# Kernel tuning notes

Measured on AMD Instinct MI355X. Metric: run time of the kernel, lower is better.

The kernel has to match this reference:

```python
import jax, jax.numpy as jnp
import numpy as np

B, C_IN, C_OUT, H, W = 4, 256, 256, 64, 64
K, STRIDE, PAD, DIL = 3, 1, 1, 1
KK = K * K


def setup_inputs() -> dict:
    key = jax.random.key(0)
    k1, k2, k3, k4 = jax.random.split(key, 4)
    x = jax.random.normal(k1, (B, C_IN, H, W), jnp.float32)
    # offset/mask conv weight (no bias), scaled small so offsets are modest
    w_mod = jax.random.normal(k2, (3 * KK, C_IN, K, K), jnp.float32) * 0.01
    # deform conv weight (xavier-ish scale) + bias
    w_def = jax.random.normal(k3, (C_OUT, C_IN, K, K), jnp.float32) * (1.0 / np.sqrt(C_IN * KK))
    b_def = jax.random.normal(k4, (C_OUT,), jnp.float32) * 0.01
    return {"x": x, "w_mod": w_mod, "w_def": w_def, "b_def": b_def}


def _conv_nchw(x, w, stride, pad):
    return jax.lax.conv_general_dilated(
        x, w, (stride, stride), [(pad, pad), (pad, pad)],
        dimension_numbers=("NCHW", "OIHW", "NCHW"))


def _bilinear_sample(x, py, px):
    # x: [B,C,H,W]; py/px: [B,KK,Ho,Wo] absolute sample coords (zero-pad outside)
    Bn, Cc, Hh, Ww = x.shape
    y0 = jnp.floor(py)
    x0 = jnp.floor(px)
    fy = py - y0
    fx = px - x0
    y0i = y0.astype(jnp.int32)
    x0i = x0.astype(jnp.int32)
    xf = x.reshape(Bn, Cc, Hh * Ww)

    def corner(yi, xi, wgt):
        valid = (yi >= 0) & (yi < Hh) & (xi >= 0) & (xi < Ww)
        yc = jnp.clip(yi, 0, Hh - 1)
        xc = jnp.clip(xi, 0, Ww - 1)
        idx = yc * Ww + xc                      # [B,KK,Ho,Wo]
        g = jax.vmap(lambda f, i: f[:, i])(xf, idx)  # [B,C,KK,Ho,Wo]
        return g * (wgt * valid)[:, None]

    return (corner(y0i, x0i, (1 - fy) * (1 - fx))
            + corner(y0i, x0i + 1, (1 - fy) * fx)
            + corner(y0i + 1, x0i, fy * (1 - fx))
            + corner(y0i + 1, x0i + 1, fy * fx))


def reference(x, w_mod, w_def, b_def):
    # offset/mask head
    mod = _conv_nchw(x, w_mod, STRIDE, PAD)          # [B, 3*KK, Ho, Wo]
    o1, o2, mask = mod[:, :KK], mod[:, KK:2 * KK], mod[:, 2 * KK:]
    offset = jnp.concatenate([o1, o2], axis=1)        # [B, 2*KK, Ho, Wo]
    # torchvision DeformConv2d: offset channels are interleaved (y, x) pairs
    dy = offset[:, 0::2]
    dx = offset[:, 1::2]
    mask = jax.nn.sigmoid(mask)                       # [B, KK, Ho, Wo]

    Ho, Wo = mod.shape[2], mod.shape[3]
    ky, kx = jnp.meshgrid(jnp.arange(K), jnp.arange(K), indexing="ij")
    ky = ky.reshape(-1).astype(jnp.float32)
    kx = kx.reshape(-1).astype(jnp.float32)
    base_y = (jnp.arange(Ho, dtype=jnp.float32) * STRIDE - PAD)[None, :, None] + (ky * DIL)[:, None, None]  # [KK,Ho,1]
    base_x = (jnp.arange(Wo, dtype=jnp.float32) * STRIDE - PAD)[None, None, :] + (kx * DIL)[:, None, None]  # [KK,1,Wo]
    py = dy + base_y[None]                            # [B,KK,Ho,Wo]
    px = dx + base_x[None]

    sampled = _bilinear_sample(x, py, px) * mask[:, None]  # [B,C,KK,Ho,Wo]
    out = jnp.einsum("bckhw,ock->bohw", sampled, w_def.reshape(C_OUT, C_IN, KK))
    return out + b_def[None, :, None, None]
```

## Files before the change

kernel.cpp:

```cpp
#include <hip/hip_runtime.h>

typedef unsigned short u16;
typedef unsigned int u32;
typedef short bf16x8 __attribute__((ext_vector_type(8)));
typedef float f32x4 __attribute__((ext_vector_type(4)));

#define CIN 256
#define COUT 256

__device__ __forceinline__ u16 f2b(float f) {
  u32 u = __float_as_uint(f);
  u += 0x7fffu + ((u >> 16) & 1u);
  return (u16)(u >> 16);
}
__device__ __forceinline__ u32 packbf(float lo, float hi) {
  return (u32)f2b(lo) | ((u32)f2b(hi) << 16);
}
__device__ __forceinline__ u32 bil2(u32 u00, u32 u01, u32 u10, u32 u11, float4 wt) {
  float s0 = __uint_as_float(u00 << 16) * wt.x;
  s0 = fmaf(__uint_as_float(u01 << 16), wt.y, s0);
  s0 = fmaf(__uint_as_float(u10 << 16), wt.z, s0);
  s0 = fmaf(__uint_as_float(u11 << 16), wt.w, s0);
  float s1 = __uint_as_float(u00 & 0xffff0000u) * wt.x;
  s1 = fmaf(__uint_as_float(u01 & 0xffff0000u), wt.y, s1);
  s1 = fmaf(__uint_as_float(u10 & 0xffff0000u), wt.z, s1);
  s1 = fmaf(__uint_as_float(u11 & 0xffff0000u), wt.w, s1);
  return packbf(s0, s1);
}
__device__ __forceinline__ void bar() {
  asm volatile("s_waitcnt lgkmcnt(0)\n\ts_barrier" ::: "memory");
}

__global__ __launch_bounds__(256) void k_prep(
    const float* __restrict__ x, const float* __restrict__ w_mod,
    const float* __restrict__ w_def,
    u16* __restrict__ xT, u16* __restrict__ Wm2, u16* __restrict__ W2) {
  __shared__ __align__(16) char SB[9216];
  int t = threadIdx.x, g = blockIdx.x;
  if (g < 1024) {
    u16 (*T)[72] = (u16(*)[72])SB;
    int b = g >> 8, ct = (g >> 6) & 3, pt = g & 63;
    int c0 = ct << 6, pos0 = pt << 6;
    {
      int cl = t >> 2, pb = (t & 3) << 4;
      const float* p = x + (((b << 8) + c0 + cl) << 12) + pos0 + pb;
#pragma unroll
      for (int i = 0; i < 4; ++i) {
        float4 v = *(const float4*)(p + i * 4);
        int pp = pb + i * 4;
        T[pp][cl] = f2b(v.x); T[pp + 1][cl] = f2b(v.y);
        T[pp + 2][cl] = f2b(v.z); T[pp + 3][cl] = f2b(v.w);
      }
    }
    __syncthreads();
    {
      int pl = t >> 2, q = t & 3;
      u16* dst = xT + (((b << 12) + pos0 + pl) << 8) + c0 + (q << 4);
      *(uint4*)dst = *(const uint4*)&T[pl][q << 4];
      *(uint4*)(dst + 8) = *(const uint4*)&T[pl][(q << 4) + 8];
    }
  } else {
    float* L = (float*)SB;
    int gg = g - 1024;
    if (gg < 256) {
      const float* src = w_def + gg * 2304;
      for (int j = t; j < 2304; j += 256) L[j] = src[j];
      __syncthreads();
      u16* dst = W2 + gg * 2304;
      for (int j = t; j < 2304; j += 256) {
        int kk = j >> 8, c = j & 255;
        dst[j] = f2b(L[c * 9 + kk]);
      }
    } else {
      int cm = gg - 256;
      if (cm < 27) {
        const float* src = w_mod + cm * 2304;
        for (int j = t; j < 2304; j += 256) L[j] = src[j];
      }
      __syncthreads();
      u16* dst = Wm2 + cm * 2304;
      for (int j = t; j < 2304; j += 256) {
        int kk = j >> 8, c = j & 255;
        dst[j] = (cm < 27) ? f2b(L[c * 9 + kk]) : (u16)0;
      }
    }
  }
}

__global__ __launch_bounds__(1024) void k_fused(
    const u16* __restrict__ xT, const u16* __restrict__ Wm2,
    const u16* __restrict__ W2, const float* __restrict__ b_def,
    float* __restrict__ out) {
  __shared__ __align__(16) char LB[107520];
  __shared__ __align__(16) int2 Ci[576];
  __shared__ __align__(16) float4 Cw[576];
  u16 (*As1)[2][64][72] = (u16 (*)[2][64][72])LB;
  float (*mods2)[32][66] = (float (*)[32][66])(LB + 73728);
  u16 (*As2)[64][72] = (u16 (*)[64][72])LB;

  int t = threadIdx.x;
  int l = t & 63;
  int w = t >> 6;
  int g = blockIdx.x;
  int b = (g & 7) >> 1, y = ((g >> 3) << 1) + (g & 1);
  const u16* xTb = xT + (b << 20);
  int ml = l & 15, kq = l >> 4;

  {
    int h = t >> 8;
    int wl = (t >> 6) & 3;
    int tg = t & 255;
    int px = tg >> 2, q = tg & 3;
    f32x4 zero = {0.f, 0.f, 0.f, 0.f};
    f32x4 acc0 = zero, acc1 = zero;
    uint4 VA0, VA1, VB0, VB1;
    uint4 S0, S1, S2, S3, T0, T1, T2, T3;

#define MC_ISSUE_A(i, V0, V1)                                                \
  { int ch_ = h * 9 + (i); int kk_ = ch_ >> 2, c0_ = (ch_ & 3) << 6;         \
    int ky_ = kk_ / 3, kx_ = kk_ - 3 * ky_;                                  \
    int ys_ = y + ky_ - 1, xs_ = px + kx_ - 1;                               \
    V0 = make_uint4(0, 0, 0, 0); V1 = V0;                                    \
    if (ys_ >= 0 && ys_ < 64 && xs_ >= 0 && xs_ < 64) {                      \
      const u16* p_ = xTb + (((ys_ << 6) + xs_) << 8) + c0_ + (q << 4);      \
      V0 = *(const uint4*)p_; V1 = *(const uint4*)(p_ + 8);                  \
    } }

#define MC_ISSUE_B(i, R0, R1, R2, R3)                                        \
  { int ch_ = h * 9 + (i); int kk_ = ch_ >> 2, c0_ = (ch_ & 3) << 6;         \
    const u16* pw_ = Wm2 + (kk_ << 8) + c0_ + (kq << 3);                     \
    R0 = *(const uint4*)(pw_ + ml * 2304);                                   \
    R1 = *(const uint4*)(pw_ + (16 + ml) * 2304);                            \
    R2 = *(const uint4*)(pw_ + ml * 2304 + 32);                              \
    R3 = *(const uint4*)(pw_ + (16 + ml) * 2304 + 32); }

#define MC_WRITE(buf, V0, V1)                                                \
  { *(uint4*)&As1[h][buf][px][q << 4] = V0;                                  \
    *(uint4*)&As1[h][buf][px][(q << 4) + 8] = V1; }

#define MC_MFMA(buf, R0, R1, R2, R3)                                         \
  { bf16x8 a0_ = *(const bf16x8*)&As1[h][buf][wl * 16 + ml][kq << 3];        \
    acc0 = __builtin_amdgcn_mfma_f32_16x16x32_bf16(a0_, *(const bf16x8*)&R0, acc0, 0,0,0); \
    acc1 = __builtin_amdgcn_mfma_f32_16x16x32_bf16(a0_, *(const bf16x8*)&R1, acc1, 0,0,0); \
    bf16x8 a1_ = *(const bf16x8*)&As1[h][buf][wl * 16 + ml][32 + (kq << 3)]; \
    acc0 = __builtin_amdgcn_mfma_f32_16x16x32_bf16(a1_, *(const bf16x8*)&R2, acc0, 0,0,0); \
    acc1 = __builtin_amdgcn_mfma_f32_16x16x32_bf16(a1_, *(const bf16x8*)&R3, acc1, 0,0,0); }

    MC_ISSUE_A(0, VA0, VA1)
    MC_ISSUE_A(1, VB0, VB1)
    MC_ISSUE_B(0, S0, S1, S2, S3)
#pragma unroll 1
    for (int i2 = 0; i2 < 8; i2 += 2) {
      MC_WRITE(0, VA0, VA1)
      bar();
      MC_ISSUE_A(i2 + 2, VA0, VA1)
      MC_ISSUE_B(i2 + 1, T0, T1, T2, T3)
      MC_MFMA(0, S0, S1, S2, S3)
      MC_WRITE(1, VB0, VB1)
      bar();
      if (i2 + 3 < 9) MC_ISSUE_A(i2 + 3, VB0, VB1)
      MC_ISSUE_B(i2 + 2, S0, S1, S2, S3)
      MC_MFMA(1, T0, T1, T2, T3)
    }
    MC_WRITE(0, VA0, VA1)
    bar();
    MC_MFMA(0, S0, S1, S2, S3)
#pragma unroll
    for (int r = 0; r < 4; ++r) {
      mods2[h][ml][wl * 16 + kq * 4 + r]      = acc0[r];
      mods2[h][16 + ml][wl * 16 + kq * 4 + r] = acc1[r];
    }
#undef MC_ISSUE_A
#undef MC_ISSUE_B
#undef MC_WRITE
#undef MC_MFMA
  }
  __syncthreads();
  if (t < 576) {
    int kk = t >> 6, pxx_i = t & 63;
    float dy = mods2[0][2 * kk][pxx_i] + mods2[1][2 * kk][pxx_i]
             + mods2[2][2 * kk][pxx_i] + mods2[3][2 * kk][pxx_i];
    float dx = mods2[0][2 * kk + 1][pxx_i] + mods2[1][2 * kk + 1][pxx_i]
             + mods2[2][2 * kk + 1][pxx_i] + mods2[3][2 * kk + 1][pxx_i];
    float mv = mods2[0][18 + kk][pxx_i] + mods2[1][18 + kk][pxx_i]
             + mods2[2][18 + kk][pxx_i] + mods2[3][18 + kk][pxx_i];
    float msk = 1.f / (1.f + __expf(-mv));
    int ky = kk / 3, kx = kk - 3 * ky;
    float py  = dy + (float)(y + ky - 1);
    float pxx = dx + (float)(pxx_i + kx - 1);
    float y0f = floorf(py), x0f = floorf(pxx);
    float fy = py - y0f, fx = pxx - x0f;
    int y0 = (int)y0f, x0 = (int)x0f;
    float vy0 = (y0 >= 0 && y0 < 64) ? msk : 0.f;
    float vy1 = (y0 + 1 >= 0 && y0 + 1 < 64) ? msk : 0.f;
    float w00 = (1.f - fy) * (1.f - fx) * vy0;
    float w01 = (1.f - fy) * fx * vy0;
    float w10 = fy * (1.f - fx) * vy1;
    float w11 = fy * fx * vy1;
    int xb2 = min(max(x0, 0), 62);
    float wA0 = (xb2 == x0) ? w00 : ((xb2 == x0 + 1) ? w01 : 0.f);
    float wB0 = (xb2 + 1 == x0) ? w00 : ((xb2 + 1 == x0 + 1) ? w01 : 0.f);
    float wA1 = (xb2 == x0) ? w10 : ((xb2 == x0 + 1) ? w11 : 0.f);
    float wB1 = (xb2 + 1 == x0) ? w10 : ((xb2 + 1 == x0 + 1) ? w11 : 0.f);
    int ib0 = min(max(y0, 0), 63) * 64 + xb2;
    int ib1 = min(max(y0 + 1, 0), 63) * 64 + xb2;
    Ci[t] = make_int2(ib0, ib1);
    Cw[t] = make_float4(wA0, wB0, wA1, wB1);
  }
  __syncthreads();

  {
    int cp = t >> 9;
    int gm = (t >> 3) & 63, go = t & 7;
    int nrow0 = (w << 4) + ml;

    f32x4 zero = {0.f, 0.f, 0.f, 0.f};
    f32x4 acc[4];
#pragma unroll
    for (int i = 0; i < 4; ++i) acc[i] = zero;

    uint4 A00, A01, A02, A03; float4 wt0;
    uint4 A10, A11, A12, A13; float4 wt1;
    uint4 SA0, SA2;
    uint4 SB0, SB2;
    uint4 TA0, TA2;
    uint4 TB0, TB2;

#define ISSUE_A(chunk, a0, a1, a2, a3, wt)                                   \
  { int kk_ = (chunk) >> 2, c0_ = ((chunk) & 3) << 6;                        \
    int cI_ = (kk_ << 6) + gm;                                               \
    int2 ib_ = Ci[cI_];                                                      \
    wt = Cw[cI_];                                                            \
    const u16* p0_ = xTb + (ib_.x << 8) + c0_ + (go << 3);                   \
    const u16* p1_ = xTb + (ib_.y << 8) + c0_ + (go << 3);                   \
    a0 = *(const uint4*)p0_;  a1 = *(const uint4*)(p0_ + 256);               \
    a2 = *(const uint4*)p1_;  a3 = *(const uint4*)(p1_ + 256); }

#define ISSUE_B(chunk, R0, R2)                                               \
  { int kk_ = (chunk) >> 2, c0_ = ((chunk) & 3) << 6;                        \
    const u16* pw_ = W2 + (kk_ << 8) + c0_ + (kq << 3);                      \
    R0 = *(const uint4*)(pw_ + nrow0 * 2304);                                \
    R2 = *(const uint4*)(pw_ + nrow0 * 2304 + 32); }

#define UNPACK(CUR, a0, a1, a2, a3, wt)                                      \
  { u32 q0_ = bil2(a0.x, a1.x, a2.x, a3.x, wt);                              \
    u32 q1_ = bil2(a0.y, a1.y, a2.y, a3.y, wt);                              \
    u32 q2_ = bil2(a0.z, a1.z, a2.z, a3.z, wt);                              \
    u32 q3_ = bil2(a0.w, a1.w, a2.w, a3.w, wt);                              \
    *(uint4*)&As2[CUR][gm][go << 3] = make_uint4(q0_, q1_, q2_, q3_); }

#define DOMFMA(CUR, R0, R2)                                                  \
  { bf16x8 a0_ = *(const bf16x8*)&As2[CUR][ml][kq << 3];                     \
    bf16x8 a1_ = *(const bf16x8*)&As2[CUR][16 + ml][kq << 3];                \
    bf16x8 a2_ = *(const bf16x8*)&As2[CUR][32 + ml][kq << 3];                \
    bf16x8 a3_ = *(const bf16x8*)&As2[CUR][48 + ml][kq << 3];                \
    bf16x8 b0_ = *(const bf16x8*)&R0;                                        \
    acc[0] = __builtin_amdgcn_mfma_f32_16x16x32_bf16(a0_, b0_, acc[0], 0,0,0); \
    acc[1] = __builtin_amdgcn_mfma_f32_16x16x32_bf16(a1_, b0_, acc[1], 0,0,0); \
    acc[2] = __builtin_amdgcn_mfma_f32_16x16x32_bf16(a2_, b0_, acc[2], 0,0,0); \
    acc[3] = __builtin_amdgcn_mfma_f32_16x16x32_bf16(a3_, b0_, acc[3], 0,0,0); \
    a0_ = *(const bf16x8*)&As2[CUR][ml][32 + (kq << 3)];                     \
    a1_ = *(const bf16x8*)&As2[CUR][16 + ml][32 + (kq << 3)];                \
    a2_ = *(const bf16x8*)&As2[CUR][32 + ml][32 + (kq << 3)];                \
    a3_ = *(const bf16x8*)&As2[CUR][48 + ml][32 + (kq << 3)];                \
    b0_ = *(const bf16x8*)&R2;                                               \
    acc[0] = __builtin_amdgcn_mfma_f32_16x16x32_bf16(a0_, b0_, acc[0], 0,0,0); \
    acc[1] = __builtin_amdgcn_mfma_f32_16x16x32_bf16(a1_, b0_, acc[1], 0,0,0); \
    acc[2] = __builtin_amdgcn_mfma_f32_16x16x32_bf16(a2_, b0_, acc[2], 0,0,0); \
    acc[3] = __builtin_amdgcn_mfma_f32_16x16x32_bf16(a3_, b0_, acc[3], 0,0,0); }

    ISSUE_A(0 + cp, A00, A01, A02, A03, wt0)
    ISSUE_A(2 + cp, A10, A11, A12, A13, wt1)
    ISSUE_B(0, SA0, SA2)
    ISSUE_B(1, SB0, SB2)
#pragma unroll 1
    for (int p2 = 0; p2 < 9; ++p2) {
      int c4 = p2 << 2;
      UNPACK(0 + cp, A00, A01, A02, A03, wt0)
      bar();
      if (p2 < 8) ISSUE_A(c4 + 4 + cp, A00, A01, A02, A03, wt0)
      ISSUE_B(c4 + 2, TA0, TA2)
      ISSUE_B(c4 + 3, TB0, TB2)
      DOMFMA(0, SA0, SA2)
      DOMFMA(1, SB0, SB2)
      UNPACK(2 + cp, A10, A11, A12, A13, wt1)
      bar();
      if (p2 < 8) {
        ISSUE_A(c4 + 6 + cp, A10, A11, A12, A13, wt1)
        ISSUE_B(c4 + 4, SA0, SA2)
        ISSUE_B(c4 + 5, SB0, SB2)
      }
      DOMFMA(2, TA0, TA2)
      DOMFMA(3, TB0, TB2)
    }

    {
      int n = nrow0;
      float bias = b_def[n];
      float* op = out + (((b << 8) + n) << 12) + (y << 6);
#pragma unroll
      for (int mt = 0; mt < 4; ++mt) {
        float4 v;
        v.x = acc[mt][0] + bias;
        v.y = acc[mt][1] + bias;
        v.z = acc[mt][2] + bias;
        v.w = acc[mt][3] + bias;
        *(float4*)(op + mt * 16 + kq * 4) = v;
      }
    }
#undef ISSUE_A
#undef ISSUE_B
#undef UNPACK
#undef DOMFMA
  }
}

extern "C" void kernel_launch(void* const* d_in, const int* in_sizes, int n_in,
                              void* d_out, int out_size, void* d_ws, size_t ws_size,
                              hipStream_t stream) {
  const float* x     = (const float*)d_in[0];
  const float* w_mod = (const float*)d_in[1];
  const float* w_def = (const float*)d_in[2];
  const float* b_def = (const float*)d_in[3];
  float* out = (float*)d_out;
  char* ws = (char*)d_ws;
  u16* xT  = (u16*)(ws);
  u16* W2  = (u16*)(ws + 8388608);
  u16* Wm2 = (u16*)(ws + 8388608 + 1179648);

  hipLaunchKernelGGL(k_prep, dim3(1312), dim3(256), 0, stream, x, w_mod, w_def, xT, Wm2, W2);
  hipLaunchKernelGGL(k_fused, dim3(256), dim3(1024), 0, stream, xT, Wm2, W2, b_def, out);
}
```

Baseline: 152.4 us.

## Re-layout deform weights per K-chunk for coalesced loads staged via LDS

The pre-pack kernel now stores the bf16 deform weights chunk-major (per kk and 64-channel slice, output rows contiguous), so each wave can fetch its 16-row weight tile as fully contiguous 16-byte loads. Before, each lane gathered strided rows. The fetched tile is written into a per-wave LDS slice and read back in MFMA operand layout. This trades scattered global loads for extra LDS writes and reads, and it relies on the per-wave LDS region not overlapping live A buffers and on intra-wave ordering without a barrier.

```diff
diff --git a/kernel.cpp b/kernel.cpp
--- a/kernel.cpp
+++ b/kernel.cpp
@@ -66,10 +66,10 @@
       const float* src = w_def + gg * 2304;
       for (int j = t; j < 2304; j += 256) L[j] = src[j];
       __syncthreads();
-      u16* dst = W2 + gg * 2304;
       for (int j = t; j < 2304; j += 256) {
         int kk = j >> 8, c = j & 255;
-        dst[j] = f2b(L[c * 9 + kk]);
+        int ch = (kk << 2) + (c >> 6), cl = c & 63;
+        W2[ch * 16384 + gg * 64 + cl] = f2b(L[c * 9 + kk]);
       }
     } else {
       int cm = gg - 256;
@@ -97,6 +97,7 @@
   u16 (*As1)[2][64][72] = (u16 (*)[2][64][72])LB;
   float (*mods2)[32][66] = (float (*)[32][66])(LB + 73728);
   u16 (*As2)[64][72] = (u16 (*)[64][72])LB;
+  u16 (*Bsl)[16][72] = (u16 (*)[16][72])(LB + 36864);
 
   int t = threadIdx.x;
   int l = t & 63;
@@ -236,11 +237,10 @@
     a0 = *(const uint4*)p0_;  a1 = *(const uint4*)(p0_ + 256);               \
     a2 = *(const uint4*)p1_;  a3 = *(const uint4*)(p1_ + 256); }
 
-#define ISSUE_B(chunk, R0, R2)                                               \
-  { int kk_ = (chunk) >> 2, c0_ = ((chunk) & 3) << 6;                        \
-    const u16* pw_ = W2 + (kk_ << 8) + c0_ + (kq << 3);                      \
-    R0 = *(const uint4*)(pw_ + nrow0 * 2304);                                \
-    R2 = *(const uint4*)(pw_ + nrow0 * 2304 + 32); }
+#define ISSUE_B(chunk, P0, P1)                                               \
+  { const u16* pw_ = W2 + (chunk) * 16384 + (w << 10) + (l << 3);            \
+    P0 = *(const uint4*)(pw_);                                               \
+    P1 = *(const uint4*)(pw_ + 512); }
 
 #define UNPACK(CUR, a0, a1, a2, a3, wt)                                      \
   { u32 q0_ = bil2(a0.x, a1.x, a2.x, a3.x, wt);                              \
@@ -249,25 +249,27 @@
     u32 q3_ = bil2(a0.w, a1.w, a2.w, a3.w, wt);                              \
     *(uint4*)&As2[CUR][gm][go << 3] = make_uint4(q0_, q1_, q2_, q3_); }
 
-#define DOMFMA(CUR, R0, R2)                                                  \
-  { bf16x8 a0_ = *(const bf16x8*)&As2[CUR][ml][kq << 3];                     \
+#define DOMFMA(CUR, P0, P1)                                                  \
+  { *(uint4*)&Bsl[w][l >> 3][(l & 7) << 3] = P0;                             \
+    *(uint4*)&Bsl[w][8 + (l >> 3)][(l & 7) << 3] = P1;                       \
+    bf16x8 b0_ = *(const bf16x8*)&Bsl[w][ml][kq << 3];                       \
+    bf16x8 a0_ = *(const bf16x8*)&As2[CUR][ml][kq << 3];                     \
     bf16x8 a1_ = *(const bf16x8*)&As2[CUR][16 + ml][kq << 3];                \
     bf16x8 a2_ = *(const bf16x8*)&As2[CUR][32 + ml][kq << 3];                \
     bf16x8 a3_ = *(const bf16x8*)&As2[CUR][48 + ml][kq << 3];                \
-    bf16x8 b0_ = *(const bf16x8*)&R0;                                        \
     acc[0] = __builtin_amdgcn_mfma_f32_16x16x32_bf16(a0_, b0_, acc[0], 0,0,0); \
     acc[1] = __builtin_amdgcn_mfma_f32_16x16x32_bf16(a1_, b0_, acc[1], 0,0,0); \
     acc[2] = __builtin_amdgcn_mfma_f32_16x16x32_bf16(a2_, b0_, acc[2], 0,0,0); \
     acc[3] = __builtin_amdgcn_mfma_f32_16x16x32_bf16(a3_, b0_, acc[3], 0,0,0); \
+    bf16x8 b1_ = *(const bf16x8*)&Bsl[w][ml][32 + (kq << 3)];                \
     a0_ = *(const bf16x8*)&As2[CUR][ml][32 + (kq << 3)];                     \
     a1_ = *(const bf16x8*)&As2[CUR][16 + ml][32 + (kq << 3)];                \
     a2_ = *(const bf16x8*)&As2[CUR][32 + ml][32 + (kq << 3)];                \
     a3_ = *(const bf16x8*)&As2[CUR][48 + ml][32 + (kq << 3)];                \
-    b0_ = *(const bf16x8*)&R2;                                               \
-    acc[0] = __builtin_amdgcn_mfma_f32_16x16x32_bf16(a0_, b0_, acc[0], 0,0,0); \
-    acc[1] = __builtin_amdgcn_mfma_f32_16x16x32_bf16(a1_, b0_, acc[1], 0,0,0); \
-    acc[2] = __builtin_amdgcn_mfma_f32_16x16x32_bf16(a2_, b0_, acc[2], 0,0,0); \
-    acc[3] = __builtin_amdgcn_mfma_f32_16x16x32_bf16(a3_, b0_, acc[3], 0,0,0); }
+    acc[0] = __builtin_amdgcn_mfma_f32_16x16x32_bf16(a0_, b1_, acc[0], 0,0,0); \
+    acc[1] = __builtin_amdgcn_mfma_f32_16x16x32_bf16(a1_, b1_, acc[1], 0,0,0); \
+    acc[2] = __builtin_amdgcn_mfma_f32_16x16x32_bf16(a2_, b1_, acc[2], 0,0,0); \
+    acc[3] = __builtin_amdgcn_mfma_f32_16x16x32_bf16(a3_, b1_, acc[3], 0,0,0); }
 
     ISSUE_A(0 + cp, A00, A01, A02, A03, wt0)
     ISSUE_A(2 + cp, A10, A11, A12, A13, wt1)
```

New measurement: 137.4 us. 9.8% less time.
